# Kernel optimization log

Hardware: AMD Instinct MI355X
Metric: run time of the kernel (lower is better)

## Reference

```python
import jax, jax.numpy as jnp
import numpy as np


def conv1x1(x, w, b):
    # x: [B,C,H,W], w: [O,C], b: [O]  (1x1 conv == per-pixel matmul)
    return jnp.einsum('oc,bchw->bohw', w, x) + b[None, :, None, None]


def setup_inputs() -> dict:
    key = jax.random.key(0)
    ks = jax.random.split(key, 8)
    B, C, H, W = 8, 256, 64, 64
    heads, points = 8, 4
    x = jax.random.normal(ks[0], (B, C, H, W), dtype=jnp.float32)
    # small offset weights so sampling grids stay mostly in-range (original inits these to 0)
    w_off = jax.random.normal(ks[1], (heads * points * 2, C), dtype=jnp.float32) * 0.01
    b_off = jax.random.normal(ks[2], (heads * points * 2,), dtype=jnp.float32) * 0.05
    w_attn = jax.random.normal(ks[3], (heads * points, C), dtype=jnp.float32) * 0.02
    b_attn = jnp.full((heads * points,), np.log(1.0 / points), dtype=jnp.float32)
    w_val = jax.random.normal(ks[4], (C, C), dtype=jnp.float32) * (1.0 / np.sqrt(C))
    b_val = jnp.zeros((C,), dtype=jnp.float32)
    w_out = jax.random.normal(ks[5], (C, C), dtype=jnp.float32) * (1.0 / np.sqrt(C))
    b_out = jnp.zeros((C,), dtype=jnp.float32)
    return {"x": x, "w_off": w_off, "b_off": b_off, "w_attn": w_attn, "b_attn": b_attn,
            "w_val": w_val, "b_val": b_val, "w_out": w_out, "b_out": b_out,
            "num_heads": heads, "num_points": points}


def _grid_sample_one(v, g):
    # v: [Cph,H,W] value image; g: [P,H,W,2] sampling grid in [-1,1] (x,y), align_corners=True,
    # bilinear, zero padding. Returns [Cph,P,H,W].
    Cph, H, W = v.shape
    ix = (g[..., 0] + 1.0) * 0.5 * (W - 1)  # [P,H,W]
    iy = (g[..., 1] + 1.0) * 0.5 * (H - 1)
    x0 = jnp.floor(ix); y0 = jnp.floor(iy)
    x1 = x0 + 1.0;      y1 = y0 + 1.0
    wx1 = ix - x0; wx0 = 1.0 - wx1
    wy1 = iy - y0; wy0 = 1.0 - wy1

    def corner(yc, xc, w):
        valid = (xc >= 0) & (xc <= W - 1) & (yc >= 0) & (yc <= H - 1)
        yi = jnp.clip(yc, 0, H - 1).astype(jnp.int32)
        xi = jnp.clip(xc, 0, W - 1).astype(jnp.int32)
        vv = v[:, yi, xi]  # [Cph,P,H,W]
        return vv * (w * valid.astype(w.dtype))[None]

    return (corner(y0, x0, wy0 * wx0) + corner(y0, x1, wy0 * wx1)
            + corner(y1, x0, wy1 * wx0) + corner(y1, x1, wy1 * wx1))


def deformable_attention(x, w_off, b_off, w_attn, b_attn, w_val, b_val, w_out, b_out,
                         num_heads, num_points):
    B, C, H, W = x.shape
    hd, P = num_heads, num_points
    cph = C // hd

    value = conv1x1(x, w_val, b_val)                       # [B,C,H,W]
    offsets = conv1x1(x, w_off, b_off)                     # [B,hd*P*2,H,W]
    attn = conv1x1(x, w_attn, b_attn).reshape(B, hd, P, H, W)
    attn = jax.nn.softmax(attn, axis=2)                    # softmax over points

    gy = jnp.linspace(-1.0, 1.0, H, dtype=x.dtype)
    gx = jnp.linspace(-1.0, 1.0, W, dtype=x.dtype)
    base = jnp.stack(jnp.meshgrid(gx, gy, indexing='xy'), axis=-1)  # [H,W,2] (x,y)

    off = offsets.reshape(B, hd, P, 2, H, W).transpose(0, 1, 2, 4, 5, 3)  # [B,hd,P,H,W,2]
    grid = base[None, None, None] + off                                   # [B,hd,P,H,W,2]

    val = value.reshape(B * hd, cph, H, W)
    grid = grid.reshape(B * hd, P, H, W, 2)
    sampled = jax.vmap(_grid_sample_one)(val, grid)        # [B*hd,cph,P,H,W]
    sampled = sampled.reshape(B, hd, cph, P, H, W)

    weighted = (sampled * attn[:, :, None]).sum(axis=3)    # [B,hd,cph,H,W]
    weighted = weighted.reshape(B, C, H, W)
    return conv1x1(weighted, w_out, b_out) + x


def reference(x, w_off, b_off, w_attn, b_attn, w_val, b_val, w_out, b_out,
              num_heads, num_points):
    return deformable_attention(x, w_off, b_off, w_attn, b_attn, w_val, b_val,
                                w_out, b_out, num_heads, num_points)
```

## Files before the change

kernel.cpp:

```cpp
#include <hip/hip_runtime.h>
#include <cstddef>

#define HW 4096
#define WPITCH 264

typedef __attribute__((ext_vector_type(8))) short short8v;
typedef __attribute__((ext_vector_type(4))) float f32x4;

__device__ inline unsigned short f2bf(float f) {
    unsigned int u = __float_as_uint(f);
    u += 0x7FFFu + ((u >> 16) & 1u);
    return (unsigned short)(u >> 16);
}
__device__ inline float bf2f(unsigned short s) {
    return __uint_as_float(((unsigned int)s) << 16);
}

__device__ inline void load_tile2(const unsigned short* __restrict__ g, int kc,
                                  int wid, int lane, short8v r[2])
{
    const int s  = lane & 7;
    const int r8 = lane >> 3;
    const unsigned short* src = g + kc + s * 8;
#pragma unroll
    for (int i = 0; i < 2; ++i) {
        const int row = wid * 16 + i * 8 + r8;
        r[i] = *(const short8v*)(src + row * 256);
    }
}

__device__ inline void store_tile2(unsigned short* lds, int wid, int lane, const short8v r[2])
{
    const int s  = lane & 7;
    const int r8 = lane >> 3;
#pragma unroll
    for (int i = 0; i < 2; ++i) {
        const int row = wid * 16 + i * 8 + r8;
        *(short8v*)((char*)lds + row * 128 + ((s ^ (row & 7)) << 4)) = r[i];
    }
}

__device__ inline short8v read_frag(const unsigned short* lds, int row, int kbyte, int lane)
{
    const char* p = (const char*)lds + row * 128 + (kbyte ^ ((lane & 7) * 16));
    return *(const short8v*)p;
}

__global__ __launch_bounds__(256)
void prep_kernel(const float* __restrict__ w_off, const float* __restrict__ b_off,
                 const float* __restrict__ w_attn, const float* __restrict__ b_attn,
                 const float* __restrict__ w_val, const float* __restrict__ b_val,
                 const float* __restrict__ w_out,
                 unsigned short* __restrict__ wcat_bf, unsigned short* __restrict__ wauxlo,
                 unsigned short* __restrict__ wout_bf, float* __restrict__ bcat)
{
    int i = blockIdx.x * 256 + threadIdx.x;
    if (i < 384 * 256) {
        int n = i >> 8, k = i & 255;
        float v;
        if (n < 256)      v = w_val[n * 256 + k];
        else if (n < 320) v = w_off[(n - 256) * 256 + k];
        else if (n < 352) v = w_attn[(n - 320) * 256 + k];
        else              v = 0.0f;
        unsigned short hi = f2bf(v);
        wcat_bf[i] = hi;
        if (n >= 256) wauxlo[(n - 256) * 256 + k] = f2bf(v - bf2f(hi));
    }
    if (i < 128 * 256) {
        int n = i >> 8;
        if (n >= 96) wauxlo[i] = 0;
    }
    if (i < 256 * 256) wout_bf[i] = f2bf(w_out[i]);
    if (i < 512) {
        float v = 0.0f;
        if (i < 256)      v = b_val[i];
        else if (i < 320) v = b_off[i - 256];
        else if (i < 352) v = b_attn[i - 320];
        bcat[i] = v;
    }
}

__global__ __launch_bounds__(256)
void transpose_kernel(const float* __restrict__ x, unsigned short* __restrict__ xhi)
{
    __shared__ float t[64][65];
    const int bid = blockIdx.x;
    const int pt = bid & 63, ct = (bid >> 6) & 3, b = bid >> 8;
    const int tid = threadIdx.x;
    const int rr = tid >> 4, c4 = (tid & 15) * 4;

    const float* src = x + ((size_t)(b * 256 + ct * 64)) * HW + pt * 64;
#pragma unroll
    for (int j = 0; j < 4; ++j) {
        float4 v = *(const float4*)&src[(size_t)(j * 16 + rr) * HW + c4];
        t[j * 16 + rr][c4 + 0] = v.x; t[j * 16 + rr][c4 + 1] = v.y;
        t[j * 16 + rr][c4 + 2] = v.z; t[j * 16 + rr][c4 + 3] = v.w;
    }
    __syncthreads();

    const size_t obase = ((size_t)b * HW + pt * 64) * 256 + ct * 64;
#pragma unroll
    for (int j = 0; j < 4; ++j) {
        int p = j * 16 + rr;
        ushort4 hi = make_ushort4(f2bf(t[c4 + 0][p]), f2bf(t[c4 + 1][p]),
                                  f2bf(t[c4 + 2][p]), f2bf(t[c4 + 3][p]));
        *(ushort4*)&xhi[obase + (size_t)p * 256 + c4] = hi;
    }
}

__device__ inline void mainloop8(const unsigned short* __restrict__ Ag,
                                 const unsigned short* __restrict__ Bg,
                                 unsigned short* Al, unsigned short* Bl,
                                 int wid, int lane, int wm, int wn, f32x4 acc[4][2])
{
    const int mloc = lane & 15, ksel = lane >> 4;
    short8v rA[2], rB[2];
    load_tile2(Ag, 0, wid, lane, rA);
    load_tile2(Bg, 0, wid, lane, rB);
#pragma unroll
    for (int kc = 0; kc < 4; ++kc) {
        if (kc) __syncthreads();
        store_tile2(Al, wid, lane, rA);
        store_tile2(Bl, wid, lane, rB);
        __syncthreads();
        if (kc < 3) {
            load_tile2(Ag, (kc + 1) * 64, wid, lane, rA);
            load_tile2(Bg, (kc + 1) * 64, wid, lane, rB);
        }
#pragma unroll
        for (int kk = 0; kk < 2; ++kk) {
            const int kb = kk * 64 + ksel * 16;
            short8v a[4], bb[2];
#pragma unroll
            for (int f = 0; f < 4; ++f) a[f]  = read_frag(Al, wm * 64 + f * 16 + mloc, kb, lane);
#pragma unroll
            for (int f = 0; f < 2; ++f) bb[f] = read_frag(Bl, wn * 32 + f * 16 + mloc, kb, lane);
#pragma unroll
            for (int fm = 0; fm < 4; ++fm)
#pragma unroll
                for (int fn = 0; fn < 2; ++fn)
                    acc[fm][fn] = __builtin_amdgcn_mfma_f32_16x16x32_bf16(a[fm], bb[fn], acc[fm][fn], 0, 0, 0);
        }
    }
}

__global__ __launch_bounds__(512)
void proj_kernel(const unsigned short* __restrict__ wcat_bf, const unsigned short* __restrict__ wauxlo,
                 const unsigned short* __restrict__ xhi, const float* __restrict__ bcat,
                 unsigned short* __restrict__ value_bf,
                 float* __restrict__ off_ws, float* __restrict__ attn_ws)
{
    __shared__ unsigned short lds[3 * 128 * 64];
    unsigned short* Al  = lds;
    unsigned short* Bl  = lds + 128 * 64;
    unsigned short* Alo = lds + 2 * 128 * 64;

    const int bid = blockIdx.x;
    const int pt = bid & 31;
    const int mt = (bid >> 5) % 3;
    const int b  = bid / 96;
    const int tid = threadIdx.x, wid = tid >> 6, lane = tid & 63;
    const int wm = wid >> 2, wn = wid & 3;
    const int mloc = lane & 15, ksel = lane >> 4;

    const unsigned short* Bg = xhi + ((size_t)b * HW + pt * 128) * 256;

    f32x4 acc[4][2];
#pragma unroll
    for (int fm = 0; fm < 4; ++fm) {
        float4 bv = *(const float4*)&bcat[mt * 128 + wm * 64 + fm * 16 + ksel * 4];
#pragma unroll
        for (int fn = 0; fn < 2; ++fn) acc[fm][fn] = (f32x4){bv.x, bv.y, bv.z, bv.w};
    }

    if (mt < 2) {
        mainloop8(wcat_bf + mt * 128 * 256, Bg, Al, Bl, wid, lane, wm, wn, acc);

#pragma unroll
        for (int fm = 0; fm < 4; ++fm) {
            const int ch = mt * 128 + wm * 64 + fm * 16 + ksel * 4;
            const int head = ch >> 5, c32 = ch & 31;
#pragma unroll
            for (int fn = 0; fn < 2; ++fn) {
                const int p = pt * 128 + wn * 32 + fn * 16 + mloc;
                f32x4 v = acc[fm][fn];
                ushort4 st = make_ushort4(f2bf(v[0]), f2bf(v[1]), f2bf(v[2]), f2bf(v[3]));
                *(ushort4*)&value_bf[(((size_t)(b * 8 + head)) * HW + p) * 32 + c32] = st;
            }
        }
    } else {
        const unsigned short* Ahg = wcat_bf + 256 * 256;
        const unsigned short* Alg = wauxlo;
        short8v rA[2], rL[2], rB[2];
        load_tile2(Ahg, 0, wid, lane, rA);
        load_tile2(Alg, 0, wid, lane, rL);
        load_tile2(Bg, 0, wid, lane, rB);
#pragma unroll
        for (int kc = 0; kc < 4; ++kc) {
            if (kc) __syncthreads();
            store_tile2(Al, wid, lane, rA);
            store_tile2(Alo, wid, lane, rL);
            store_tile2(Bl, wid, lane, rB);
            __syncthreads();
            if (kc < 3) {
                load_tile2(Ahg, (kc + 1) * 64, wid, lane, rA);
                load_tile2(Alg, (kc + 1) * 64, wid, lane, rL);
                load_tile2(Bg, (kc + 1) * 64, wid, lane, rB);
            }
#pragma unroll
            for (int kk = 0; kk < 2; ++kk) {
                const int kb = kk * 64 + ksel * 16;
                short8v ah[4], al[4], bb[2];
#pragma unroll
                for (int f = 0; f < 4; ++f) {
                    ah[f] = read_frag(Al,  wm * 64 + f * 16 + mloc, kb, lane);
                    al[f] = read_frag(Alo, wm * 64 + f * 16 + mloc, kb, lane);
                }
#pragma unroll
                for (int f = 0; f < 2; ++f) bb[f] = read_frag(Bl, wn * 32 + f * 16 + mloc, kb, lane);
#pragma unroll
                for (int fm = 0; fm < 4; ++fm)
#pragma unroll
                    for (int fn = 0; fn < 2; ++fn) {
                        acc[fm][fn] = __builtin_amdgcn_mfma_f32_16x16x32_bf16(ah[fm], bb[fn], acc[fm][fn], 0, 0, 0);
                        acc[fm][fn] = __builtin_amdgcn_mfma_f32_16x16x32_bf16(al[fm], bb[fn], acc[fm][fn], 0, 0, 0);
                    }
            }
        }
#pragma unroll
        for (int fm = 0; fm < 4; ++fm) {
            const int ch0 = wm * 64 + fm * 16 + ksel * 4;
#pragma unroll
            for (int fn = 0; fn < 2; ++fn) {
                const int p = pt * 128 + wn * 32 + fn * 16 + mloc;
                f32x4 v = acc[fm][fn];
                if (ch0 < 64) {
                    *(float4*)&off_ws[((size_t)b * HW + p) * 64 + ch0] =
                        make_float4(v[0], v[1], v[2], v[3]);
                } else if (ch0 < 96) {
                    float m  = fmaxf(fmaxf(v[0], v[1]), fmaxf(v[2], v[3]));
                    float e0 = __expf(v[0] - m), e1 = __expf(v[1] - m);
                    float e2 = __expf(v[2] - m), e3 = __expf(v[3] - m);
                    float inv = 1.0f / (e0 + e1 + e2 + e3);
                    *(float4*)&attn_ws[((size_t)b * HW + p) * 32 + (ch0 - 64)] =
                        make_float4(e0 * inv, e1 * inv, e2 * inv, e3 * inv);
                }
            }
        }
    }
}

__global__ __launch_bounds__(512)
void sampleout_kernel(const unsigned short* __restrict__ value_bf,
                      const float* __restrict__ off_ws, const float* __restrict__ attn_ws,
                      const unsigned short* __restrict__ wout_bf, const float* __restrict__ b_out,
                      const float* __restrict__ x, float* __restrict__ out)
{
    __shared__ unsigned short Wp[64 * WPITCH];
    __shared__ unsigned short Asm[256 * 64];

    const int bid = blockIdx.x;
    const int pt = bid & 63, b = bid >> 6;
    const int tid = threadIdx.x;

    {
        const int c4     = tid & 7;
        const int posIdx = tid >> 3;
        const int p      = pt * 64 + posIdx;
        const int h      = p >> 6;
        const int w      = p & 63;
        const float gx = w * (2.0f / 63.0f) - 1.0f;
        const float gy = h * (2.0f / 63.0f) - 1.0f;

        const float* awp  = attn_ws + ((size_t)b * HW + p) * 32;
        const float* offp = off_ws + ((size_t)b * HW + p) * 64;

#pragma unroll
        for (int head = 0; head < 8; ++head) {
            float4 aw4 = *(const float4*)&awp[head * 4];
            float aw[4] = {aw4.x, aw4.y, aw4.z, aw4.w};
            float4 o01 = *(const float4*)&offp[head * 8];
            float4 o23 = *(const float4*)&offp[head * 8 + 4];
            float oxv[4] = {o01.x, o01.z, o23.x, o23.z};
            float oyv[4] = {o01.y, o01.w, o23.y, o23.w};

            float4 acc = make_float4(0.f, 0.f, 0.f, 0.f);
            const unsigned short* vb = value_bf + (size_t)(b * 8 + head) * HW * 32 + c4 * 4;
#pragma unroll
            for (int ptq = 0; ptq < 4; ++ptq) {
                float ix = (gx + oxv[ptq] + 1.0f) * 31.5f;
                float iy = (gy + oyv[ptq] + 1.0f) * 31.5f;
                float x0f = floorf(ix), y0f = floorf(iy);
                float wx1 = ix - x0f, wx0 = 1.0f - wx1;
                float wy1 = iy - y0f, wy0 = 1.0f - wy1;
                int x0 = (int)x0f, y0 = (int)y0f;
                int x1 = x0 + 1,   y1 = y0 + 1;
                float a = aw[ptq];
                float vx0 = (x0 >= 0 && x0 <= 63) ? 1.f : 0.f;
                float vx1 = (x1 >= 0 && x1 <= 63) ? 1.f : 0.f;
                float vy0 = (y0 >= 0 && y0 <= 63) ? 1.f : 0.f;
                float vy1 = (y1 >= 0 && y1 <= 63) ? 1.f : 0.f;
                float w00 = a * wy0 * wx0 * vy0 * vx0;
                float w01 = a * wy0 * wx1 * vy0 * vx1;
                float w10 = a * wy1 * wx0 * vy1 * vx0;
                float w11 = a * wy1 * wx1 * vy1 * vx1;
                int cx0 = min(max(x0, 0), 63), cx1 = min(max(x1, 0), 63);
                int cy0 = min(max(y0, 0), 63), cy1 = min(max(y1, 0), 63);
                ushort4 u00 = *(const ushort4*)&vb[(size_t)(cy0 * 64 + cx0) * 32];
                ushort4 u01 = *(const ushort4*)&vb[(size_t)(cy0 * 64 + cx1) * 32];
                ushort4 u10 = *(const ushort4*)&vb[(size_t)(cy1 * 64 + cx0) * 32];
                ushort4 u11 = *(const ushort4*)&vb[(size_t)(cy1 * 64 + cx1) * 32];
                acc.x += w00 * bf2f(u00.x) + w01 * bf2f(u01.x) + w10 * bf2f(u10.x) + w11 * bf2f(u11.x);
                acc.y += w00 * bf2f(u00.y) + w01 * bf2f(u01.y) + w10 * bf2f(u10.y) + w11 * bf2f(u11.y);
                acc.z += w00 * bf2f(u00.z) + w01 * bf2f(u01.z) + w10 * bf2f(u10.z) + w11 * bf2f(u11.z);
                acc.w += w00 * bf2f(u00.w) + w01 * bf2f(u01.w) + w10 * bf2f(u10.w) + w11 * bf2f(u11.w);
            }
            const int slot = head * 4 + (c4 >> 1);
            const int byte = posIdx * (WPITCH * 2) + ((slot ^ (posIdx & 7)) << 4) + (c4 & 1) * 8;
            ushort4 st = make_ushort4(f2bf(acc.x), f2bf(acc.y), f2bf(acc.z), f2bf(acc.w));
            *(ushort4*)((char*)Wp + byte) = st;
        }
    }
    __syncthreads();

    const int wid = tid >> 6, lane = tid & 63;
    const int wm = wid & 3, wn = wid >> 2;
    const int mloc = lane & 15, ksel = lane >> 4;
    const int s = lane & 7, r8 = lane >> 3;

    f32x4 acc2[4][2];
#pragma unroll
    for (int fm = 0; fm < 4; ++fm)
#pragma unroll
        for (int fn = 0; fn < 2; ++fn) acc2[fm][fn] = (f32x4){0.f, 0.f, 0.f, 0.f};

    short8v rA[4];
#pragma unroll
    for (int i = 0; i < 4; ++i)
        rA[i] = *(const short8v*)(wout_bf + (wid * 32 + i * 8 + r8) * 256 + s * 8);

#pragma unroll
    for (int kc = 0; kc < 4; ++kc) {
        if (kc) __syncthreads();
#pragma unroll
        for (int i = 0; i < 4; ++i) {
            const int row = wid * 32 + i * 8 + r8;
            *(short8v*)((char*)Asm + row * 128 + ((s ^ (row & 7)) << 4)) = rA[i];
        }
        __syncthreads();
        if (kc < 3) {
#pragma unroll
            for (int i = 0; i < 4; ++i)
                rA[i] = *(const short8v*)(wout_bf + (wid * 32 + i * 8 + r8) * 256 + (kc + 1) * 64 + s * 8);
        }
#pragma unroll
        for (int kk = 0; kk < 2; ++kk) {
            short8v a[4], bb[2];
#pragma unroll
            for (int f = 0; f < 4; ++f) {
                const int row = wm * 64 + f * 16 + mloc;
                a[f] = *(const short8v*)((char*)Asm + row * 128 + (((kk * 4 + ksel) ^ (row & 7)) << 4));
            }
#pragma unroll
            for (int f = 0; f < 2; ++f) {
                const int row = wn * 32 + f * 16 + mloc;
                const int slot = kc * 8 + kk * 4 + ksel;
                bb[f] = *(const short8v*)((char*)Wp + row * (WPITCH * 2) + ((slot ^ (row & 7)) << 4));
            }
#pragma unroll
            for (int fm = 0; fm < 4; ++fm)
#pragma unroll
                for (int fn = 0; fn < 2; ++fn)
                    acc2[fm][fn] = __builtin_amdgcn_mfma_f32_16x16x32_bf16(a[fm], bb[fn], acc2[fm][fn], 0, 0, 0);
        }
    }

#pragma unroll
    for (int fm = 0; fm < 4; ++fm) {
        const int o = wm * 64 + fm * 16 + ksel * 4;
        float4 bo = *(const float4*)&b_out[o];
#pragma unroll
        for (int fn = 0; fn < 2; ++fn) {
            const int p = pt * 64 + wn * 32 + fn * 16 + mloc;
            const size_t idx = ((size_t)(b * 256 + o)) * HW + p;
            f32x4 v = acc2[fm][fn];
            out[idx + 0 * HW] = v[0] + bo.x + x[idx + 0 * HW];
            out[idx + 1 * HW] = v[1] + bo.y + x[idx + 1 * HW];
            out[idx + 2 * HW] = v[2] + bo.z + x[idx + 2 * HW];
            out[idx + 3 * HW] = v[3] + bo.w + x[idx + 3 * HW];
        }
    }
}

extern "C" void kernel_launch(void* const* d_in, const int* in_sizes, int n_in,
                              void* d_out, int out_size, void* d_ws, size_t ws_size,
                              hipStream_t stream)
{
    const float* x      = (const float*)d_in[0];
    const float* w_off  = (const float*)d_in[1];
    const float* b_off  = (const float*)d_in[2];
    const float* w_attn = (const float*)d_in[3];
    const float* b_attn = (const float*)d_in[4];
    const float* w_val  = (const float*)d_in[5];
    const float* b_val  = (const float*)d_in[6];
    const float* w_out  = (const float*)d_in[7];
    const float* b_out  = (const float*)d_in[8];
    float* out = (float*)d_out;

    char* ws = (char*)d_ws;
    unsigned short* wcat_bf = (unsigned short*)(ws + 0);
    unsigned short* wauxlo  = (unsigned short*)(ws + 196608);
    unsigned short* wout_bf = (unsigned short*)(ws + 262144);
    float*          bcat    = (float*)(ws + 393216);
    unsigned short* xhi     = (unsigned short*)(ws + 395264);
    unsigned short* val_bf  = (unsigned short*)(ws + 17172480);
    float*          off_ws  = (float*)(ws + 33949696);
    float*          attn_ws = (float*)(ws + 42338304);

    prep_kernel<<<384, 256, 0, stream>>>(w_off, b_off, w_attn, b_attn, w_val, b_val,
                                         w_out, wcat_bf, wauxlo, wout_bf, bcat);
    transpose_kernel<<<2048, 256, 0, stream>>>(x, xhi);
    proj_kernel<<<768, 512, 0, stream>>>(wcat_bf, wauxlo, xhi, bcat, val_bf, off_ws, attn_ws);
    sampleout_kernel<<<512, 512, 0, stream>>>(val_bf, off_ws, attn_ws, wout_bf, b_out, x, out);
}
```

Measured before the change: 72.14 us.

## Halve sampleout tile to 32 positions and split heads across thread pairs

The sample+output-projection kernel now processes 32 pixel positions per block instead of 64 and launches 1024 blocks instead of 512. Each position is handled by 16 threads, with the two halves of each group covering four heads apiece, so sampling work per thread is halved. The MFMA stage shrinks to one N-fragment per wave. The aim is more parallelism, with 1024 blocks on 256 CUs, and shorter per-block latency. The cost is that each block reloads the full W_out matrix for half as many positions, doubling redundant weight traffic and staging per output.

```diff
diff --git a/kernel.cpp b/kernel.cpp
--- a/kernel.cpp
+++ b/kernel.cpp
@@ -250,23 +250,24 @@
     }
 }
 
-__global__ __launch_bounds__(512)
+__global__ __launch_bounds__(512, 1)
 void sampleout_kernel(const unsigned short* __restrict__ value_bf,
                       const float* __restrict__ off_ws, const float* __restrict__ attn_ws,
                       const unsigned short* __restrict__ wout_bf, const float* __restrict__ b_out,
                       const float* __restrict__ x, float* __restrict__ out)
 {
-    __shared__ unsigned short Wp[64 * WPITCH];
+    __shared__ unsigned short Wp[32 * WPITCH];
     __shared__ unsigned short Asm[256 * 64];
 
     const int bid = blockIdx.x;
-    const int pt = bid & 63, b = bid >> 6;
+    const int pt = bid & 127, b = bid >> 7;
     const int tid = threadIdx.x;
 
     {
         const int c4     = tid & 7;
-        const int posIdx = tid >> 3;
-        const int p      = pt * 64 + posIdx;
+        const int hh     = (tid >> 3) & 1;
+        const int posIdx = tid >> 4;
+        const int p      = pt * 32 + posIdx;
         const int h      = p >> 6;
         const int w      = p & 63;
         const float gx = w * (2.0f / 63.0f) - 1.0f;
@@ -276,7 +277,8 @@
         const float* offp = off_ws + ((size_t)b * HW + p) * 64;
 
 #pragma unroll
-        for (int head = 0; head < 8; ++head) {
+        for (int hq = 0; hq < 4; ++hq) {
+            const int head = hh * 4 + hq;
             float4 aw4 = *(const float4*)&awp[head * 4];
             float aw[4] = {aw4.x, aw4.y, aw4.z, aw4.w};
             float4 o01 = *(const float4*)&offp[head * 8];
@@ -328,11 +330,9 @@
     const int mloc = lane & 15, ksel = lane >> 4;
     const int s = lane & 7, r8 = lane >> 3;
 
-    f32x4 acc2[4][2];
-#pragma unroll
-    for (int fm = 0; fm < 4; ++fm)
-#pragma unroll
-        for (int fn = 0; fn < 2; ++fn) acc2[fm][fn] = (f32x4){0.f, 0.f, 0.f, 0.f};
+    f32x4 acc2[4];
+#pragma unroll
+    for (int fm = 0; fm < 4; ++fm) acc2[fm] = (f32x4){0.f, 0.f, 0.f, 0.f};
 
     short8v rA[4];
 #pragma unroll
@@ -355,23 +355,20 @@
         }
 #pragma unroll
         for (int kk = 0; kk < 2; ++kk) {
-            short8v a[4], bb[2];
+            short8v a[4], bb;
 #pragma unroll
             for (int f = 0; f < 4; ++f) {
                 const int row = wm * 64 + f * 16 + mloc;
                 a[f] = *(const short8v*)((char*)Asm + row * 128 + (((kk * 4 + ksel) ^ (row & 7)) << 4));
             }
-#pragma unroll
-            for (int f = 0; f < 2; ++f) {
-                const int row = wn * 32 + f * 16 + mloc;
+            {
+                const int row = wn * 16 + mloc;
                 const int slot = kc * 8 + kk * 4 + ksel;
-                bb[f] = *(const short8v*)((char*)Wp + row * (WPITCH * 2) + ((slot ^ (row & 7)) << 4));
+                bb = *(const short8v*)((char*)Wp + row * (WPITCH * 2) + ((slot ^ (row & 7)) << 4));
             }
 #pragma unroll
             for (int fm = 0; fm < 4; ++fm)
-#pragma unroll
-                for (int fn = 0; fn < 2; ++fn)
-                    acc2[fm][fn] = __builtin_amdgcn_mfma_f32_16x16x32_bf16(a[fm], bb[fn], acc2[fm][fn], 0, 0, 0);
+                acc2[fm] = __builtin_amdgcn_mfma_f32_16x16x32_bf16(a[fm], bb, acc2[fm], 0, 0, 0);
         }
     }
 
@@ -379,16 +376,13 @@
     for (int fm = 0; fm < 4; ++fm) {
         const int o = wm * 64 + fm * 16 + ksel * 4;
         float4 bo = *(const float4*)&b_out[o];
-#pragma unroll
-        for (int fn = 0; fn < 2; ++fn) {
-            const int p = pt * 64 + wn * 32 + fn * 16 + mloc;
-            const size_t idx = ((size_t)(b * 256 + o)) * HW + p;
-            f32x4 v = acc2[fm][fn];
-            out[idx + 0 * HW] = v[0] + bo.x + x[idx + 0 * HW];
-            out[idx + 1 * HW] = v[1] + bo.y + x[idx + 1 * HW];
-            out[idx + 2 * HW] = v[2] + bo.z + x[idx + 2 * HW];
-            out[idx + 3 * HW] = v[3] + bo.w + x[idx + 3 * HW];
-        }
+        const int p = pt * 32 + wn * 16 + mloc;
+        const size_t idx = ((size_t)(b * 256 + o)) * HW + p;
+        f32x4 v = acc2[fm];
+        out[idx + 0 * HW] = v[0] + bo.x + x[idx + 0 * HW];
+        out[idx + 1 * HW] = v[1] + bo.y + x[idx + 1 * HW];
+        out[idx + 2 * HW] = v[2] + bo.z + x[idx + 2 * HW];
+        out[idx + 3 * HW] = v[3] + bo.w + x[idx + 3 * HW];
     }
 }
 
@@ -421,5 +415,5 @@
                                          w_out, wcat_bf, wauxlo, wout_bf, bcat);
     transpose_kernel<<<2048, 256, 0, stream>>>(x, xhi);
     proj_kernel<<<768, 512, 0, stream>>>(wcat_bf, wauxlo, xhi, bcat, val_bf, off_ws, attn_ws);
-    sampleout_kernel<<<512, 512, 0, stream>>>(val_bf, off_ws, attn_ws, wout_bf, b_out, x, out);
-}
+    sampleout_kernel<<<1024, 512, 0, stream>>>(val_bf, off_ws, attn_ws, wout_bf, b_out, x, out);
+}
```

New measurement: 73.54 us. No clear change (+1.9%).
